# Kernel tuning notes

Measured on AMD Instinct MI355X. Metric: run time of the kernel, lower is better.

The kernel has to match this reference:

```python
import jax, jax.numpy as jnp
import numpy as np

N, E, G = 50000, 400000, 64
IN_C, HID, OUT_C, HEADS = 256, 128, 256, 4
LRELU_SLOPE = 0.2
LN_EPS = 1e-5


def setup_inputs() -> dict:
    key = jax.random.key(0)
    ks = jax.random.split(key, 16)
    d = {}
    d["x"] = jax.random.normal(ks[0], (N, IN_C), dtype=jnp.float32)
    d["edge_index"] = jax.random.randint(ks[1], (2, E), 0, N, dtype=jnp.int32)
    d["batch"] = jnp.sort(jax.random.randint(ks[2], (N,), 0, G, dtype=jnp.int32))
    s1 = 1.0 / np.sqrt(IN_C)
    d["W1"] = jax.random.uniform(ks[3], (IN_C, HEADS * HID), jnp.float32, -s1, s1)
    d["att_src1"] = jax.random.normal(ks[4], (HEADS, HID), jnp.float32) * 0.1
    d["att_dst1"] = jax.random.normal(ks[5], (HEADS, HID), jnp.float32) * 0.1
    d["b1"] = jnp.zeros((HEADS * HID,), jnp.float32)
    d["ln1_g"] = jnp.ones((HEADS * HID,), jnp.float32)
    d["ln1_b"] = jnp.zeros((HEADS * HID,), jnp.float32)
    s2 = 1.0 / np.sqrt(HEADS * HID)
    d["W2"] = jax.random.uniform(ks[6], (HEADS * HID, OUT_C), jnp.float32, -s2, s2)
    d["att_src2"] = jax.random.normal(ks[7], (1, OUT_C), jnp.float32) * 0.1
    d["att_dst2"] = jax.random.normal(ks[8], (1, OUT_C), jnp.float32) * 0.1
    d["b2"] = jnp.zeros((OUT_C,), jnp.float32)
    d["ln2_g"] = jnp.ones((OUT_C,), jnp.float32)
    d["ln2_b"] = jnp.zeros((OUT_C,), jnp.float32)
    return d


def _layernorm(x, g, b):
    mu = jnp.mean(x, axis=-1, keepdims=True)
    var = jnp.mean(jnp.square(x - mu), axis=-1, keepdims=True)
    return (x - mu) * jax.lax.rsqrt(var + LN_EPS) * g + b


def _gat_conv(x, src, dst, W, a_src, a_dst, bias):
    # PyG GATConv (eval mode, dropout inactive), self-loops already in src/dst.
    H, C = a_src.shape
    h = (x @ W).reshape(N, H, C)                       # [N,H,C]
    e_src = jnp.einsum('nhc,hc->nh', h, a_src)          # [N,H]
    e_dst = jnp.einsum('nhc,hc->nh', h, a_dst)
    e = jax.nn.leaky_relu(e_src[src] + e_dst[dst], LRELU_SLOPE)  # [Etot,H]
    m = jax.ops.segment_max(e, dst, num_segments=N)     # segment softmax over incoming edges
    ex = jnp.exp(e - m[dst])
    s = jax.ops.segment_sum(ex, dst, num_segments=N)
    alpha = ex / (s[dst] + 1e-16)                       # [Etot,H]
    msg = h[src] * alpha[:, :, None]                    # [Etot,H,C]
    out = jax.ops.segment_sum(msg, dst, num_segments=N) # [N,H,C]
    return out.reshape(N, H * C) + bias


def reference(x, edge_index, batch, W1, att_src1, att_dst1, b1, ln1_g, ln1_b,
              W2, att_src2, att_dst2, b2, ln2_g, ln2_b):
    loops = jnp.arange(N, dtype=edge_index.dtype)
    src = jnp.concatenate([edge_index[0], loops])
    dst = jnp.concatenate([edge_index[1], loops])
    h = _gat_conv(x, src, dst, W1, att_src1, att_dst1, b1)
    h = _layernorm(h, ln1_g, ln1_b)
    h = jax.nn.relu(h)                                  # dropout is identity in eval
    h = _gat_conv(h, src, dst, W2, att_src2, att_dst2, b2)
    h = _layernorm(h, ln2_g, ln2_b)
    # global_mean_pool over graphs
    sums = jax.ops.segment_sum(h, batch, num_segments=G)
    cnts = jax.ops.segment_sum(jnp.ones((N,), h.dtype), batch, num_segments=G)
    return sums / jnp.maximum(cnts, 1.0)[:, None]
```

## Files before the change

kernel.cpp:

```cpp
#include <hip/hip_runtime.h>
#include <hip/hip_bf16.h>
#include <cstdint>

#define LRELU_SLOPE 0.2f

typedef short bf16x8 __attribute__((ext_vector_type(8)));
typedef float f32x4  __attribute__((ext_vector_type(4)));

__device__ __forceinline__ float b2f(unsigned short u) {
  return __uint_as_float(((unsigned int)u) << 16);
}
__device__ __forceinline__ unsigned short f2b(float f) {
  unsigned int u = __float_as_uint(f);
  return (unsigned short)((u + 0x7fff + ((u >> 16) & 1)) >> 16);
}

__device__ __forceinline__ void gload16(const void* g, void* l) {
  __builtin_amdgcn_global_load_lds(
      (const __attribute__((address_space(1))) unsigned int*)g,
      (__attribute__((address_space(3))) unsigned int*)l, 16, 0, 0);
}

__global__ __launch_bounds__(256)
void cvt_bf16_pad(const float* __restrict__ x, unsigned short* __restrict__ o,
                  int M, int D, int Mpad) {
  const int i = blockIdx.x * 256 + threadIdx.x;
  const int per_row = D / 4;
  if (i >= Mpad * per_row) return;
  const int row = i / per_row;
  const int c4  = (i % per_row) * 4;
  ushort4 v = make_ushort4(0, 0, 0, 0);
  if (row < M) {
    const float4 f = *(const float4*)&x[(size_t)row * D + c4];
    v = make_ushort4(f2b(f.x), f2b(f.y), f2b(f.z), f2b(f.w));
  }
  *(ushort4*)&o[(size_t)row * D + c4] = v;
}

__global__ __launch_bounds__(256)
void cvt_wt(const float* __restrict__ W, unsigned short* __restrict__ WT,
            int K, int N) {
  const int j = blockIdx.x * 256 + threadIdx.x;
  if (j >= N * K) return;
  const int n = j / K, k = j % K;
  WT[j] = f2b(W[(size_t)k * N + n]);
}

__global__ __launch_bounds__(256)
void csr_count(const int* __restrict__ ei, int E, int Etot,
               int* __restrict__ count) {
  const int i = blockIdx.x * 256 + threadIdx.x;
  if (i >= Etot) return;
  const int d = (i < E) ? ei[E + i] : (i - E);
  atomicAdd(&count[d], 1);
}

__global__ __launch_bounds__(256)
void scan_blocksum(const int* __restrict__ count, int* __restrict__ bsum, int Nn) {
  const int i0 = blockIdx.x * 1024 + threadIdx.x * 4;
  int s = 0;
#pragma unroll
  for (int k = 0; k < 4; ++k) { const int i = i0 + k; if (i < Nn) s += count[i]; }
#pragma unroll
  for (int off = 1; off < 64; off <<= 1) s += __shfl_xor(s, off);
  __shared__ int ws[4];
  if ((threadIdx.x & 63) == 0) ws[threadIdx.x >> 6] = s;
  __syncthreads();
  if (threadIdx.x == 0) bsum[blockIdx.x] = ws[0] + ws[1] + ws[2] + ws[3];
}

__global__ __launch_bounds__(64)
void scan_top(const int* __restrict__ bsum, int* __restrict__ boff,
              int* __restrict__ rowptrN, int nb) {
  const int t = threadIdx.x;
  const int v = (t < nb) ? bsum[t] : 0;
  int incl = v;
#pragma unroll
  for (int off = 1; off < 64; off <<= 1) {
    const int u = __shfl_up(incl, off);
    if (t >= off) incl += u;
  }
  if (t < nb) boff[t] = incl - v;
  if (t == 63) *rowptrN = incl;
}

__global__ __launch_bounds__(256)
void scan_apply(const int* __restrict__ count, const int* __restrict__ boff,
                int* __restrict__ rowptr, int* __restrict__ cursor, int Nn) {
  const int t = threadIdx.x;
  const int lane = t & 63;
  const int w = t >> 6;
  const int i0 = blockIdx.x * 1024 + t * 4;
  int c[4]; int s = 0;
#pragma unroll
  for (int k = 0; k < 4; ++k) { const int i = i0 + k; c[k] = (i < Nn) ? count[i] : 0; s += c[k]; }
  int incl = s;
#pragma unroll
  for (int off = 1; off < 64; off <<= 1) {
    const int u = __shfl_up(incl, off);
    if (lane >= off) incl += u;
  }
  __shared__ int ws[4];
  if (lane == 63) ws[w] = incl;
  __syncthreads();
  int woff = 0;
  for (int k = 0; k < w; ++k) woff += ws[k];
  int base = boff[blockIdx.x] + woff + incl - s;
#pragma unroll
  for (int k = 0; k < 4; ++k) {
    const int i = i0 + k;
    if (i < Nn) { rowptr[i] = base; cursor[i] = base; base += c[k]; }
  }
}

__global__ __launch_bounds__(256)
void csr_scatter(const int* __restrict__ ei, int E, int Etot,
                 int* __restrict__ cursor, int* __restrict__ srcs) {
  const int i = blockIdx.x * 256 + threadIdx.x;
  if (i >= Etot) return;
  const int s = (i < E) ? ei[i]     : (i - E);
  const int d = (i < E) ? ei[E + i] : (i - E);
  const int pos = atomicAdd(&cursor[d], 1);
  srcs[pos] = s;
}

template<int KSTEPS>
__global__ __launch_bounds__(256)
void gemm_bf16(const unsigned short* __restrict__ A,
               const unsigned short* __restrict__ BT,
               unsigned short* __restrict__ C, int M, int Nn, int K) {
  __shared__ unsigned short As[2][128 * 32];
  __shared__ unsigned short Bs[2][128 * 32];
  const int tid  = threadIdx.x;
  const int lane = tid & 63;
  const int wave = tid >> 6;
  const int wm = wave >> 1, wn = wave & 1;
  const int brow = blockIdx.y * 128;
  const int bcol = blockIdx.x * 128;
  const int srow  = tid >> 2;
  const int sslot = tid & 3;
  const int sswz  = sslot ^ (srow & 3);
  const size_t aBase0 = (size_t)(brow + srow) * K + sswz * 8;
  const size_t aBase1 = (size_t)(brow + 64 + srow) * K + sswz * 8;
  const size_t bBase0 = (size_t)(bcol + srow) * K + sswz * 8;
  const size_t bBase1 = (size_t)(bcol + 64 + srow) * K + sswz * 8;
  const int ldsOff0 = srow * 32 + sslot * 8;
  const int ldsOff1 = (64 + srow) * 32 + sslot * 8;

  f32x4 acc[4][4] = {};
  const int u   = lane >> 4;
  const int r15 = lane & 15;
  const int sw  = u ^ (r15 & 3);

  auto stage = [&](int buf, int ks) {
    const int k0 = ks * 32;
    gload16(A + aBase0 + k0, &As[buf][ldsOff0]);
    gload16(A + aBase1 + k0, &As[buf][ldsOff1]);
    gload16(BT + bBase0 + k0, &Bs[buf][ldsOff0]);
    gload16(BT + bBase1 + k0, &Bs[buf][ldsOff1]);
  };

  stage(0, 0);
  asm volatile("s_waitcnt vmcnt(0)" ::: "memory");
  __syncthreads();
  int cur = 0;
#pragma unroll
  for (int ks = 0; ks < KSTEPS; ++ks) {
    if (ks + 1 < KSTEPS) stage(cur ^ 1, ks + 1);
    bf16x8 af[4], bfv[4];
#pragma unroll
    for (int m = 0; m < 4; ++m) {
      const int row = wm * 64 + m * 16 + r15;
      af[m]  = *(const bf16x8*)&As[cur][row * 32 + sw * 8];
      const int col = wn * 64 + m * 16 + r15;
      bfv[m] = *(const bf16x8*)&Bs[cur][col * 32 + sw * 8];
    }
#pragma unroll
    for (int m = 0; m < 4; ++m)
#pragma unroll
      for (int n = 0; n < 4; ++n)
        acc[m][n] = __builtin_amdgcn_mfma_f32_16x16x32_bf16(
            af[m], bfv[n], acc[m][n], 0, 0, 0);
    if (ks + 1 < KSTEPS) {
      asm volatile("s_waitcnt vmcnt(0)" ::: "memory");
      __syncthreads();
      cur ^= 1;
    }
  }
#pragma unroll
  for (int m = 0; m < 4; ++m) {
    const int r0 = brow + wm * 64 + m * 16 + u * 4;
#pragma unroll
    for (int n = 0; n < 4; ++n) {
      const int cc = bcol + wn * 64 + n * 16 + r15;
#pragma unroll
      for (int r = 0; r < 4; ++r)
        if (r0 + r < M) C[(size_t)(r0 + r) * Nn + cc] = f2b(acc[m][n][r]);
    }
  }
}

template<int H, int C>
__global__ __launch_bounds__(H * C / 4)
void node_att(const unsigned short* __restrict__ h,
              const float* __restrict__ a_src, const float* __restrict__ a_dst,
              float* __restrict__ es, float* __restrict__ ed) {
  const int n = blockIdx.x;
  const int t = threadIdx.x;
  const int c4 = t * 4;
  const int head = c4 / C;
  const ushort4 hv = *(const ushort4*)&h[(size_t)n * (H * C) + c4];
  const float4 as = *(const float4*)&a_src[c4];
  const float4 ad = *(const float4*)&a_dst[c4];
  const float x0 = b2f(hv.x), x1 = b2f(hv.y), x2 = b2f(hv.z), x3 = b2f(hv.w);
  float ps = x0 * as.x + x1 * as.y + x2 * as.z + x3 * as.w;
  float pd = x0 * ad.x + x1 * ad.y + x2 * ad.z + x3 * ad.w;
#pragma unroll
  for (int off = C / 8; off >= 1; off >>= 1) {
    ps += __shfl_xor(ps, off);
    pd += __shfl_xor(pd, off);
  }
  if ((t & (C / 4 - 1)) == 0) {
    es[n * H + head] = ps;
    ed[n * H + head] = pd;
  }
}

template<int H, int C, bool RELU, bool BFOUT>
__global__ __launch_bounds__(256)
void gat_agg_ln(const int* __restrict__ rowptr, const int* __restrict__ srcs,
                const unsigned short* __restrict__ h, const float* __restrict__ es,
                const float* __restrict__ ed, const float* __restrict__ bias,
                const float* __restrict__ lng, const float* __restrict__ lnb,
                unsigned short* __restrict__ obf, float* __restrict__ of32,
                int Nn) {
  constexpr int HC = H * C;
  constexpr int F  = HC / 64;
  const int wave = threadIdx.x >> 6;
  const int lane = threadIdx.x & 63;
  const int n = blockIdx.x * 4 + wave;
  if (n >= Nn) return;
  const int beg = rowptr[n];
  const int deg = rowptr[n + 1] - beg;

  const int myh = lane & (H - 1);
  const float edv = ed[n * H + myh];
  float ssum = 0.f;
  for (int it = lane; it < deg * H; it += 64) {
    const int j = (H == 4) ? (it >> 2) : it;
    const int src = srcs[beg + j];
    float e = es[src * H + myh] + edv;
    e = (e > 0.f) ? e : LRELU_SLOPE * e;
    ssum += __expf(e);
  }
#pragma unroll
  for (int off = H; off < 64; off <<= 1) ssum += __shfl_xor(ssum, off);

  const int hl = (lane * F) / C;
  const float inv_s = 1.0f / (__shfl(ssum, hl) + 1e-16f);
  const float edh = ed[n * H + hl];

  float acc[F];
#pragma unroll
  for (int i = 0; i < F; ++i) acc[i] = 0.f;

  auto get_alpha = [&](int src) {
    float e = es[src * H + hl] + edh;
    e = (e > 0.f) ? e : LRELU_SLOPE * e;
    return __expf(e) * inv_s;
  };
  auto fma_rows = [&](const ushort4* v0, const ushort4* v1, const float* a, int cnt) {
    for (int q = 0; q < cnt; ++q) {
      acc[0] = fmaf(b2f(v0[q].x), a[q], acc[0]);
      acc[1] = fmaf(b2f(v0[q].y), a[q], acc[1]);
      acc[2] = fmaf(b2f(v0[q].z), a[q], acc[2]);
      acc[3] = fmaf(b2f(v0[q].w), a[q], acc[3]);
      if constexpr (F == 8) {
        acc[4] = fmaf(b2f(v1[q].x), a[q], acc[4]);
        acc[5] = fmaf(b2f(v1[q].y), a[q], acc[5]);
        acc[6] = fmaf(b2f(v1[q].z), a[q], acc[6]);
        acc[7] = fmaf(b2f(v1[q].w), a[q], acc[7]);
      }
    }
  };

  int j = 0;
  for (; j + 4 <= deg; j += 4) {
    int s4[4];
#pragma unroll
    for (int q = 0; q < 4; ++q) s4[q] = srcs[beg + j + q];
    ushort4 v0[4], v1[4];
#pragma unroll
    for (int q = 0; q < 4; ++q) {
      const unsigned short* hp = &h[(size_t)s4[q] * HC + lane * F];
      v0[q] = *(const ushort4*)hp;
      if constexpr (F == 8) v1[q] = *(const ushort4*)(hp + 4);
    }
    float a4[4];
#pragma unroll
    for (int q = 0; q < 4; ++q) a4[q] = get_alpha(s4[q]);
    fma_rows(v0, v1, a4, 4);
  }
  for (; j < deg; ++j) {
    const int src = srcs[beg + j];
    const unsigned short* hp = &h[(size_t)src * HC + lane * F];
    ushort4 v0 = *(const ushort4*)hp, v1;
    if constexpr (F == 8) v1 = *(const ushort4*)(hp + 4);
    const float a = get_alpha(src);
    fma_rows(&v0, &v1, &a, 1);
  }

#pragma unroll
  for (int i = 0; i < F; i += 4) {
    const float4 bb = *(const float4*)&bias[lane * F + i];
    acc[i + 0] += bb.x; acc[i + 1] += bb.y;
    acc[i + 2] += bb.z; acc[i + 3] += bb.w;
  }
  float sum = 0.f, sq = 0.f;
#pragma unroll
  for (int i = 0; i < F; ++i) { sum += acc[i]; sq += acc[i] * acc[i]; }
#pragma unroll
  for (int off = 1; off < 64; off <<= 1) {
    sum += __shfl_xor(sum, off);
    sq  += __shfl_xor(sq, off);
  }
  const float mu  = sum / HC;
  const float var = sq / HC - mu * mu;
  const float r   = rsqrtf(var + 1e-5f);
  float y[F];
#pragma unroll
  for (int i = 0; i < F; i += 4) {
    const float4 gg = *(const float4*)&lng[lane * F + i];
    const float4 bl = *(const float4*)&lnb[lane * F + i];
    y[i + 0] = (acc[i + 0] - mu) * r * gg.x + bl.x;
    y[i + 1] = (acc[i + 1] - mu) * r * gg.y + bl.y;
    y[i + 2] = (acc[i + 2] - mu) * r * gg.z + bl.z;
    y[i + 3] = (acc[i + 3] - mu) * r * gg.w + bl.w;
  }
  if constexpr (RELU) {
#pragma unroll
    for (int i = 0; i < F; ++i) y[i] = fmaxf(y[i], 0.f);
  }
  if constexpr (BFOUT) {
    unsigned short* op = &obf[(size_t)n * HC + lane * F];
    *(ushort4*)op = make_ushort4(f2b(y[0]), f2b(y[1]), f2b(y[2]), f2b(y[3]));
    if constexpr (F == 8)
      *(ushort4*)(op + 4) = make_ushort4(f2b(y[4]), f2b(y[5]), f2b(y[6]), f2b(y[7]));
  } else {
    float* op = &of32[(size_t)n * HC + lane * F];
    *(float4*)op = make_float4(y[0], y[1], y[2], y[3]);
    if constexpr (F == 8)
      *(float4*)(op + 4) = make_float4(y[4], y[5], y[6], y[7]);
  }
}

__global__ __launch_bounds__(256)
void pool_partial(const unsigned short* __restrict__ x, const int* __restrict__ batch,
                  float* __restrict__ tmp, int* __restrict__ cnt, int Nn) {
  const int r0 = blockIdx.x * 64;
  const int rend = min(r0 + 64, Nn);
  const int t = threadIdx.x;
  float acc = 0.f;
  int cur = batch[r0];
  int seglen = 0;
  for (int r = r0; r < rend; ++r) {
    const int g = batch[r];
    if (g != cur) {
      unsafeAtomicAdd(&tmp[cur * 256 + t], acc);
      if (t == 0) atomicAdd(&cnt[cur], seglen);
      acc = 0.f; seglen = 0; cur = g;
    }
    acc += b2f(x[(size_t)r * 256 + t]);
    ++seglen;
  }
  unsafeAtomicAdd(&tmp[cur * 256 + t], acc);
  if (t == 0) atomicAdd(&cnt[cur], seglen);
}

__global__ __launch_bounds__(256)
void pool_final(const float* __restrict__ tmp, const int* __restrict__ cnt,
                float* __restrict__ out) {
  const int g = blockIdx.x;
  const int t = threadIdx.x;
  out[g * 256 + t] = tmp[g * 256 + t] / fmaxf((float)cnt[g], 1.f);
}

extern "C" void kernel_launch(void* const* d_in, const int* in_sizes, int n_in,
                              void* d_out, int out_size, void* d_ws, size_t ws_size,
                              hipStream_t stream) {
  const float* x    = (const float*)d_in[0];
  const int*   ei   = (const int*)d_in[1];
  const int*   batch= (const int*)d_in[2];
  const float* W1   = (const float*)d_in[3];
  const float* as1  = (const float*)d_in[4];
  const float* ad1  = (const float*)d_in[5];
  const float* b1   = (const float*)d_in[6];
  const float* g1   = (const float*)d_in[7];
  const float* be1  = (const float*)d_in[8];
  const float* W2   = (const float*)d_in[9];
  const float* as2  = (const float*)d_in[10];
  const float* ad2  = (const float*)d_in[11];
  const float* b2   = (const float*)d_in[12];
  const float* g2   = (const float*)d_in[13];
  const float* be2  = (const float*)d_in[14];

  const int N    = in_sizes[0] / 256;
  const int E    = in_sizes[1] / 2;
  const int Etot = E + N;
  const int Mpad = ((N + 127) / 128) * 128;
  const int NB   = (N + 1023) / 1024;

  float* ws = (float*)d_ws;
  unsigned short* out2 = (unsigned short*)ws;
  unsigned short* A2bf = out2 + (size_t)N * 256;
  unsigned short* A1bf = A2bf;
  unsigned short* h1bf = A2bf + (size_t)Mpad * 512;
  unsigned short* W1T  = h1bf + (size_t)N * 512;
  unsigned short* W2T  = W1T + 512 * 256;
  float* es   = (float*)(W2T + 512 * 256);
  float* ed   = es + (size_t)N * 4;
  int* count  = (int*)(ed + (size_t)N * 4);
  int* rowptr = count + N;
  int* cursor = rowptr + N + 1;
  int* srcs   = cursor + N;
  float* ptmp = (float*)(srcs + Etot);
  int*   pcnt = (int*)(ptmp + 64 * 256);
  int*   bsum = pcnt + 64;
  int*   boff = bsum + 64;
  unsigned short* h2bf = h1bf;

  const int eb = (Etot + 255) / 256;

  hipMemsetAsync(count, 0, (size_t)N * 4, stream);
  hipMemsetAsync(ptmp, 0, (size_t)(64 * 256 + 64) * 4, stream);
  hipMemsetAsync(A2bf + (size_t)N * 512, 0, (size_t)(Mpad - N) * 512 * 2, stream);

  csr_count<<<eb, 256, 0, stream>>>(ei, E, Etot, count);
  scan_blocksum<<<NB, 256, 0, stream>>>(count, bsum, N);
  scan_top<<<1, 64, 0, stream>>>(bsum, boff, &rowptr[N], NB);
  scan_apply<<<NB, 256, 0, stream>>>(count, boff, rowptr, cursor, N);
  csr_scatter<<<eb, 256, 0, stream>>>(ei, E, Etot, cursor, srcs);

  cvt_bf16_pad<<<((size_t)Mpad * 64 + 255) / 256, 256, 0, stream>>>(x, A1bf, N, 256, Mpad);
  cvt_wt<<<(512 * 256 + 255) / 256, 256, 0, stream>>>(W1, W1T, 256, 512);
  cvt_wt<<<(512 * 256 + 255) / 256, 256, 0, stream>>>(W2, W2T, 512, 256);

  gemm_bf16<8><<<dim3(4, Mpad / 128), 256, 0, stream>>>(A1bf, W1T, h1bf, N, 512, 256);
  node_att<4, 128><<<N, 128, 0, stream>>>(h1bf, as1, ad1, es, ed);
  gat_agg_ln<4, 128, true, true><<<(N + 3) / 4, 256, 0, stream>>>(
      rowptr, srcs, h1bf, es, ed, b1, g1, be1, A2bf, nullptr, N);

  gemm_bf16<16><<<dim3(2, Mpad / 128), 256, 0, stream>>>(A2bf, W2T, h2bf, N, 256, 512);
  node_att<1, 256><<<N, 64, 0, stream>>>(h2bf, as2, ad2, es, ed);
  gat_agg_ln<1, 256, false, true><<<(N + 3) / 4, 256, 0, stream>>>(
      rowptr, srcs, h2bf, es, ed, b2, g2, be2, out2, nullptr, N);

  pool_partial<<<(N + 63) / 64, 256, 0, stream>>>(out2, batch, ptmp, pcnt, N);
  pool_final<<<64, 256, 0, stream>>>(ptmp, pcnt, (float*)d_out);
}
```

Measured before the change: 318.5 us.

## Fuse attention scores into GEMM epilogue and precompute edge exp weights

```diff
diff --git a/kernel.cpp b/kernel.cpp
--- a/kernel.cpp
+++ b/kernel.cpp
@@ -22,37 +22,38 @@
 }
 
 __global__ __launch_bounds__(256)
-void cvt_bf16_pad(const float* __restrict__ x, unsigned short* __restrict__ o,
-                  int M, int D, int Mpad) {
+void prep_x_count(const float* __restrict__ x, unsigned short* __restrict__ o,
+                  int M, int Mpad, const int* __restrict__ ei, int E, int Etot,
+                  int* __restrict__ count) {
   const int i = blockIdx.x * 256 + threadIdx.x;
-  const int per_row = D / 4;
-  if (i >= Mpad * per_row) return;
-  const int row = i / per_row;
-  const int c4  = (i % per_row) * 4;
-  ushort4 v = make_ushort4(0, 0, 0, 0);
-  if (row < M) {
-    const float4 f = *(const float4*)&x[(size_t)row * D + c4];
-    v = make_ushort4(f2b(f.x), f2b(f.y), f2b(f.z), f2b(f.w));
-  }
-  *(ushort4*)&o[(size_t)row * D + c4] = v;
-}
-
-__global__ __launch_bounds__(256)
-void cvt_wt(const float* __restrict__ W, unsigned short* __restrict__ WT,
-            int K, int N) {
-  const int j = blockIdx.x * 256 + threadIdx.x;
-  if (j >= N * K) return;
-  const int n = j / K, k = j % K;
-  WT[j] = f2b(W[(size_t)k * N + n]);
-}
-
-__global__ __launch_bounds__(256)
-void csr_count(const int* __restrict__ ei, int E, int Etot,
-               int* __restrict__ count) {
-  const int i = blockIdx.x * 256 + threadIdx.x;
-  if (i >= Etot) return;
-  const int d = (i < E) ? ei[E + i] : (i - E);
-  atomicAdd(&count[d], 1);
+  if (i < Mpad * 64) {
+    const int row = i >> 6;
+    const int c4  = (i & 63) * 4;
+    ushort4 v = make_ushort4(0, 0, 0, 0);
+    if (row < M) {
+      const float4 f = *(const float4*)&x[(size_t)row * 256 + c4];
+      v = make_ushort4(f2b(f.x), f2b(f.y), f2b(f.z), f2b(f.w));
+    }
+    *(ushort4*)&o[(size_t)row * 256 + c4] = v;
+  }
+  if (i < Etot) {
+    const int d = (i < E) ? ei[E + i] : (i - E);
+    atomicAdd(&count[d], 1);
+  }
+}
+
+__global__ __launch_bounds__(256)
+void cvt_wts(const float* __restrict__ W1, const float* __restrict__ W2,
+             unsigned short* __restrict__ W1T, unsigned short* __restrict__ W2T) {
+  int j = blockIdx.x * 256 + threadIdx.x;
+  if (j < 512 * 256) {
+    const int n = j >> 8, k = j & 255;
+    W1T[j] = f2b(W1[(size_t)k * 512 + n]);
+  } else {
+    j -= 512 * 256;
+    const int n = j >> 9, k = j & 511;
+    W2T[j] = f2b(W2[(size_t)k * 256 + n]);
+  }
 }
 
 __global__ __launch_bounds__(256)
@@ -115,20 +116,25 @@
 
 __global__ __launch_bounds__(256)
 void csr_scatter(const int* __restrict__ ei, int E, int Etot,
-                 int* __restrict__ cursor, int* __restrict__ srcs) {
+                 int* __restrict__ cursor, int* __restrict__ srcs,
+                 int* __restrict__ dsts) {
   const int i = blockIdx.x * 256 + threadIdx.x;
   if (i >= Etot) return;
   const int s = (i < E) ? ei[i]     : (i - E);
   const int d = (i < E) ? ei[E + i] : (i - E);
   const int pos = atomicAdd(&cursor[d], 1);
   srcs[pos] = s;
+  dsts[pos] = d;
 }
 
 template<int KSTEPS>
 __global__ __launch_bounds__(256)
 void gemm_bf16(const unsigned short* __restrict__ A,
                const unsigned short* __restrict__ BT,
-               unsigned short* __restrict__ C, int M, int Nn, int K) {
+               unsigned short* __restrict__ C, int M, int Nn, int K,
+               const float* __restrict__ asrc, const float* __restrict__ adst,
+               float* __restrict__ es, float* __restrict__ ed,
+               int H, int lgC) {
   __shared__ unsigned short As[2][128 * 32];
   __shared__ unsigned short Bs[2][128 * 32];
   const int tid  = threadIdx.x;
@@ -198,42 +204,80 @@
         if (r0 + r < M) C[(size_t)(r0 + r) * Nn + cc] = f2b(acc[m][n][r]);
     }
   }
-}
-
-template<int H, int C>
-__global__ __launch_bounds__(H * C / 4)
-void node_att(const unsigned short* __restrict__ h,
-              const float* __restrict__ a_src, const float* __restrict__ a_dst,
-              float* __restrict__ es, float* __restrict__ ed) {
-  const int n = blockIdx.x;
-  const int t = threadIdx.x;
-  const int c4 = t * 4;
-  const int head = c4 / C;
-  const ushort4 hv = *(const ushort4*)&h[(size_t)n * (H * C) + c4];
-  const float4 as = *(const float4*)&a_src[c4];
-  const float4 ad = *(const float4*)&a_dst[c4];
-  const float x0 = b2f(hv.x), x1 = b2f(hv.y), x2 = b2f(hv.z), x3 = b2f(hv.w);
-  float ps = x0 * as.x + x1 * as.y + x2 * as.z + x3 * as.w;
-  float pd = x0 * ad.x + x1 * ad.y + x2 * ad.z + x3 * ad.w;
-#pragma unroll
-  for (int off = C / 8; off >= 1; off >>= 1) {
-    ps += __shfl_xor(ps, off);
-    pd += __shfl_xor(pd, off);
-  }
-  if ((t & (C / 4 - 1)) == 0) {
-    es[n * H + head] = ps;
-    ed[n * H + head] = pd;
+  const int head = bcol >> lgC;
+  float asv[4], adv[4];
+#pragma unroll
+  for (int n = 0; n < 4; ++n) {
+    const int cc = bcol + wn * 64 + n * 16 + r15;
+    asv[n] = asrc[cc];
+    adv[n] = adst[cc];
+  }
+#pragma unroll
+  for (int m = 0; m < 4; ++m) {
+#pragma unroll
+    for (int r = 0; r < 4; ++r) {
+      float pes = 0.f, ped = 0.f;
+#pragma unroll
+      for (int n = 0; n < 4; ++n) {
+        pes = fmaf(acc[m][n][r], asv[n], pes);
+        ped = fmaf(acc[m][n][r], adv[n], ped);
+      }
+#pragma unroll
+      for (int off = 1; off < 16; off <<= 1) {
+        pes += __shfl_xor(pes, off);
+        ped += __shfl_xor(ped, off);
+      }
+      if (r15 == 0) {
+        const int row = brow + wm * 64 + m * 16 + u * 4 + r;
+        if (row < M) {
+          unsafeAtomicAdd(&es[row * H + head], pes);
+          unsafeAtomicAdd(&ed[row * H + head], ped);
+        }
+      }
+    }
+  }
+}
+
+template<int H>
+__global__ __launch_bounds__(256)
+void ex_compute(const int* __restrict__ srcs, const int* __restrict__ dsts,
+                const float* __restrict__ es, const float* __restrict__ ed,
+                float* __restrict__ exCSR, float* __restrict__ s, int Etot) {
+  const int p = blockIdx.x * 256 + threadIdx.x;
+  if (p >= Etot) return;
+  const int sN = srcs[p], dN = dsts[p];
+  if constexpr (H == 4) {
+    const float4 a = *(const float4*)&es[sN * 4];
+    const float4 b = *(const float4*)&ed[dN * 4];
+    float4 v;
+    float e0 = a.x + b.x, e1 = a.y + b.y, e2 = a.z + b.z, e3 = a.w + b.w;
+    e0 = (e0 > 0.f) ? e0 : LRELU_SLOPE * e0;
+    e1 = (e1 > 0.f) ? e1 : LRELU_SLOPE * e1;
+    e2 = (e2 > 0.f) ? e2 : LRELU_SLOPE * e2;
+    e3 = (e3 > 0.f) ? e3 : LRELU_SLOPE * e3;
+    v.x = __expf(e0); v.y = __expf(e1); v.z = __expf(e2); v.w = __expf(e3);
+    *(float4*)&exCSR[p * 4] = v;
+    unsafeAtomicAdd(&s[dN * 4 + 0], v.x);
+    unsafeAtomicAdd(&s[dN * 4 + 1], v.y);
+    unsafeAtomicAdd(&s[dN * 4 + 2], v.z);
+    unsafeAtomicAdd(&s[dN * 4 + 3], v.w);
+  } else {
+    float e = es[sN] + ed[dN];
+    e = (e > 0.f) ? e : LRELU_SLOPE * e;
+    const float v = __expf(e);
+    exCSR[p] = v;
+    unsafeAtomicAdd(&s[dN], v);
   }
 }
 
 template<int H, int C, bool RELU, bool BFOUT>
 __global__ __launch_bounds__(256)
 void gat_agg_ln(const int* __restrict__ rowptr, const int* __restrict__ srcs,
-                const unsigned short* __restrict__ h, const float* __restrict__ es,
-                const float* __restrict__ ed, const float* __restrict__ bias,
-                const float* __restrict__ lng, const float* __restrict__ lnb,
-                unsigned short* __restrict__ obf, float* __restrict__ of32,
-                int Nn) {
+                const float* __restrict__ exCSR, const float* __restrict__ s,
+                const unsigned short* __restrict__ h,
+                const float* __restrict__ bias, const float* __restrict__ lng,
+                const float* __restrict__ lnb, unsigned short* __restrict__ obf,
+                float* __restrict__ of32, int Nn) {
   constexpr int HC = H * C;
   constexpr int F  = HC / 64;
   const int wave = threadIdx.x >> 6;
@@ -242,33 +286,13 @@
   if (n >= Nn) return;
   const int beg = rowptr[n];
   const int deg = rowptr[n + 1] - beg;
-
-  const int myh = lane & (H - 1);
-  const float edv = ed[n * H + myh];
-  float ssum = 0.f;
-  for (int it = lane; it < deg * H; it += 64) {
-    const int j = (H == 4) ? (it >> 2) : it;
-    const int src = srcs[beg + j];
-    float e = es[src * H + myh] + edv;
-    e = (e > 0.f) ? e : LRELU_SLOPE * e;
-    ssum += __expf(e);
-  }
-#pragma unroll
-  for (int off = H; off < 64; off <<= 1) ssum += __shfl_xor(ssum, off);
-
   const int hl = (lane * F) / C;
-  const float inv_s = 1.0f / (__shfl(ssum, hl) + 1e-16f);
-  const float edh = ed[n * H + hl];
+  const float inv_s = 1.0f / (s[n * H + hl] + 1e-16f);
 
   float acc[F];
 #pragma unroll
   for (int i = 0; i < F; ++i) acc[i] = 0.f;
 
-  auto get_alpha = [&](int src) {
-    float e = es[src * H + hl] + edh;
-    e = (e > 0.f) ? e : LRELU_SLOPE * e;
-    return __expf(e) * inv_s;
-  };
   auto fma_rows = [&](const ushort4* v0, const ushort4* v1, const float* a, int cnt) {
     for (int q = 0; q < cnt; ++q) {
       acc[0] = fmaf(b2f(v0[q].x), a[q], acc[0]);
@@ -287,8 +311,11 @@
   int j = 0;
   for (; j + 4 <= deg; j += 4) {
     int s4[4];
+    float a4[4];
 #pragma unroll
     for (int q = 0; q < 4; ++q) s4[q] = srcs[beg + j + q];
+#pragma unroll
+    for (int q = 0; q < 4; ++q) a4[q] = exCSR[(beg + j + q) * H + hl] * inv_s;
     ushort4 v0[4], v1[4];
 #pragma unroll
     for (int q = 0; q < 4; ++q) {
@@ -296,17 +323,14 @@
       v0[q] = *(const ushort4*)hp;
       if constexpr (F == 8) v1[q] = *(const ushort4*)(hp + 4);
     }
-    float a4[4];
-#pragma unroll
-    for (int q = 0; q < 4; ++q) a4[q] = get_alpha(s4[q]);
     fma_rows(v0, v1, a4, 4);
   }
   for (; j < deg; ++j) {
     const int src = srcs[beg + j];
+    const float a = exCSR[(beg + j) * H + hl] * inv_s;
     const unsigned short* hp = &h[(size_t)src * HC + lane * F];
     ushort4 v0 = *(const ushort4*)hp, v1;
     if constexpr (F == 8) v1 = *(const ushort4*)(hp + 4);
-    const float a = get_alpha(src);
     fma_rows(&v0, &v1, &a, 1);
   }
 
@@ -417,13 +441,19 @@
   unsigned short* h1bf = A2bf + (size_t)Mpad * 512;
   unsigned short* W1T  = h1bf + (size_t)N * 512;
   unsigned short* W2T  = W1T + 512 * 256;
-  float* es   = (float*)(W2T + 512 * 256);
-  float* ed   = es + (size_t)N * 4;
-  int* count  = (int*)(ed + (size_t)N * 4);
+  float* es1 = (float*)(W2T + 512 * 256);
+  float* ed1 = es1 + (size_t)N * 4;
+  float* s1  = ed1 + (size_t)N * 4;
+  float* es2 = s1  + (size_t)N * 4;
+  float* ed2 = es2 + N;
+  float* s2  = ed2 + N;
+  int* count  = (int*)(s2 + N);
   int* rowptr = count + N;
   int* cursor = rowptr + N + 1;
   int* srcs   = cursor + N;
-  float* ptmp = (float*)(srcs + Etot);
+  int* dsts   = srcs + Etot;
+  float* exCSR = (float*)(dsts + Etot);
+  float* ptmp = exCSR + (size_t)Etot * 4;
   int*   pcnt = (int*)(ptmp + 64 * 256);
   int*   bsum = pcnt + 64;
   int*   boff = bsum + 64;
@@ -431,29 +461,30 @@
 
   const int eb = (Etot + 255) / 256;
 
-  hipMemsetAsync(count, 0, (size_t)N * 4, stream);
+  hipMemsetAsync(es1, 0, (size_t)N * 15 * 4 + (size_t)N * 4, stream);
   hipMemsetAsync(ptmp, 0, (size_t)(64 * 256 + 64) * 4, stream);
   hipMemsetAsync(A2bf + (size_t)N * 512, 0, (size_t)(Mpad - N) * 512 * 2, stream);
 
-  csr_count<<<eb, 256, 0, stream>>>(ei, E, Etot, count);
+  prep_x_count<<<(Mpad * 64 + 255) / 256, 256, 0, stream>>>(
+      x, A1bf, N, Mpad, ei, E, Etot, count);
+  cvt_wts<<<(2 * 512 * 256 + 255) / 256, 256, 0, stream>>>(W1, W2, W1T, W2T);
+
   scan_blocksum<<<NB, 256, 0, stream>>>(count, bsum, N);
   scan_top<<<1, 64, 0, stream>>>(bsum, boff, &rowptr[N], NB);
   scan_apply<<<NB, 256, 0, stream>>>(count, boff, rowptr, cursor, N);
-  csr_scatter<<<eb, 256, 0, stream>>>(ei, E, Etot, cursor, srcs);
-
-  cvt_bf16_pad<<<((size_t)Mpad * 64 + 255) / 256, 256, 0, stream>>>(x, A1bf, N, 256, Mpad);
-  cvt_wt<<<(512 * 256 + 255) / 256, 256, 0, stream>>>(W1, W1T, 256, 512);
-  cvt_wt<<<(512 * 256 + 255) / 256, 256, 0, stream>>>(W2, W2T, 512, 256);
-
-  gemm_bf16<8><<<dim3(4, Mpad / 128), 256, 0, stream>>>(A1bf, W1T, h1bf, N, 512, 256);
-  node_att<4, 128><<<N, 128, 0, stream>>>(h1bf, as1, ad1, es, ed);
+  csr_scatter<<<eb, 256, 0, stream>>>(ei, E, Etot, cursor, srcs, dsts);
+
+  gemm_bf16<8><<<dim3(4, Mpad / 128), 256, 0, stream>>>(
+      A1bf, W1T, h1bf, N, 512, 256, as1, ad1, es1, ed1, 4, 7);
+  ex_compute<4><<<eb, 256, 0, stream>>>(srcs, dsts, es1, ed1, exCSR, s1, Etot);
   gat_agg_ln<4, 128, true, true><<<(N + 3) / 4, 256, 0, stream>>>(
-      rowptr, srcs, h1bf, es, ed, b1, g1, be1, A2bf, nullptr, N);
-
-  gemm_bf16<16><<<dim3(2, Mpad / 128), 256, 0, stream>>>(A2bf, W2T, h2bf, N, 256, 512);
-  node_att<1, 256><<<N, 64, 0, stream>>>(h2bf, as2, ad2, es, ed);
+      rowptr, srcs, exCSR, s1, h1bf, b1, g1, be1, A2bf, nullptr, N);
+
+  gemm_bf16<16><<<dim3(2, Mpad / 128), 256, 0, stream>>>(
+      A2bf, W2T, h2bf, N, 256, 512, as2, ad2, es2, ed2, 1, 8);
+  ex_compute<1><<<eb, 256, 0, stream>>>(srcs, dsts, es2, ed2, exCSR, s2, Etot);
   gat_agg_ln<1, 256, false, true><<<(N + 3) / 4, 256, 0, stream>>>(
-      rowptr, srcs, h2bf, es, ed, b2, g2, be2, out2, nullptr, N);
+      rowptr, srcs, exCSR, s2, h2bf, b2, g2, be2, out2, nullptr, N);
 
   pool_partial<<<(N + 63) / 64, 256, 0, stream>>>(out2, batch, ptmp, pcnt, N);
   pool_final<<<64, 256, 0, stream>>>(ptmp, pcnt, (float*)d_out);
```

Result: slower. 455.7 us (+43.1%).
